# Kernel optimization log

Measured on AMD Instinct MI355X. Metric: run time of the kernel, lower is better.

The kernel has to match this reference:

```python
import jax, jax.numpy as jnp
import numpy as np

N_QUBITS = 8
N_LAYERS = 3
BN_EPS = 1e-5


def _apply_ry(state, theta, wire):
    # state: (B, 2, ..., 2) real statevector; theta: scalar or (B,)
    st = jnp.moveaxis(state, wire + 1, 1)
    t = jnp.asarray(theta, state.dtype)
    t = t.reshape(t.shape + (1,) * (state.ndim - 2))  # broadcast vs (B, 2^{n-1})
    c, s = jnp.cos(t / 2), jnp.sin(t / 2)
    s0, s1 = st[:, 0], st[:, 1]
    new = jnp.stack([c * s0 - s * s1, s * s0 + c * s1], axis=1)
    return jnp.moveaxis(new, 1, wire + 1)


def _apply_cnot(state, ctrl, tgt):
    # assumes ctrl < tgt (chain topology used by the circuit)
    st = jnp.moveaxis(state, ctrl + 1, 1)
    a0, a1 = st[:, 0], st[:, 1]
    a1 = jnp.flip(a1, axis=tgt)  # target axis is tgt after removing the ctrl axis
    new = jnp.stack([a0, a1], axis=1)
    return jnp.moveaxis(new, 1, ctrl + 1)


def _circuit(enc_angles, params):
    # Batched 8-qubit statevector simulation; RY/CNOT are real so the state is real.
    B = enc_angles.shape[0]
    state = jnp.zeros((B, 2 ** N_QUBITS), enc_angles.dtype).at[:, 0].set(1.0)
    state = state.reshape((B,) + (2,) * N_QUBITS)
    for i in range(4):  # feature-map encoder on first 4 wires
        state = _apply_ry(state, enc_angles[:, i], i)
    for layer in range(N_LAYERS):
        for q in range(N_QUBITS):
            state = _apply_ry(state, params[layer, q], q)
        for q in range(N_QUBITS - 1):
            state = _apply_cnot(state, q, q + 1)
    probs = state * state
    ez = []
    for w in range(N_QUBITS):
        axes = tuple(a for a in range(1, N_QUBITS + 1) if a != w + 1)
        p = probs.sum(axis=axes)  # (B, 2)
        ez.append(p[:, 0] - p[:, 1])  # <Z_w>
    return jnp.stack(ez, axis=-1)  # (B, N_QUBITS)


def setup_inputs() -> dict:
    key = jax.random.key(0)
    k1, k2, k3, k4 = jax.random.split(key, 4)
    B = 65536
    return {
        "x": jax.random.normal(k1, (B, 1, 12, 12), dtype=jnp.float32),
        "params": jax.random.normal(k2, (N_LAYERS, N_QUBITS), dtype=jnp.float32),
        "W": jax.random.normal(k3, (4, N_QUBITS), dtype=jnp.float32) * 0.3,
        "b": jax.random.normal(k4, (4,), dtype=jnp.float32) * 0.1,
        "gamma": jnp.ones((4,), dtype=jnp.float32),
        "beta": jnp.zeros((4,), dtype=jnp.float32),
    }


def reference(x, params, W, b, gamma, beta):
    B = x.shape[0]
    # avg_pool2d(kernel_size=6) on 12x12 -> 2x2, then flatten to 4 encoding angles
    pooled = x.reshape(B, 1, 2, 6, 2, 6).mean(axis=(3, 5)).reshape(B, 4)
    q_out = _circuit(pooled, params)          # (B, 8)
    out = q_out @ W.T + b                      # Linear(8 -> 4)
    mean = out.mean(axis=0)                    # BatchNorm1d training mode
    var = out.var(axis=0)                      # biased variance (torch BN)
    return gamma * (out - mean) / jnp.sqrt(var + BN_EPS) + beta
```

## Files before the change

### kernel.cpp

```cpp
#include <hip/hip_runtime.h>
#include <math.h>

#define NQ 8
#define NS 256
#define NK 16
#define NL 3
#define MTS 260

__global__ __launch_bounds__(256) void setup_kernel(
    const float* __restrict__ params,
    const float* __restrict__ W,
    float* __restrict__ R_ws,
    double* __restrict__ acc)
{
    __shared__ float M[NS * NK];
    __shared__ float MT[NK * MTS];
    __shared__ float PT[NK * MTS];
    const int t = threadIdx.x;
    const int j = blockIdx.x;

    if (j == 0) acc[t] = 0.0;

    #pragma unroll
    for (int k = 0; k < NK; ++k) M[t * NK + k] = 0.f;
    if ((t & 15) == 0) M[t * NK + (t >> 4)] = 1.f;

    const int pair = t & 127;
    const int kh   = t >> 7;

    for (int layer = 0; layer < NL; ++layer) {
        for (int q = 0; q < NQ; ++q) {
            __syncthreads();
            const float th = params[layer * 8 + q] * 0.5f;
            const float c  = __cosf(th);
            const float sn = __sinf(th);
            const int m   = 1 << (7 - q);
            const int low = pair & (m - 1);
            const int s0  = ((pair ^ low) << 1) | low;
            const int s1  = s0 | m;
            float v0[8], v1[8];
            #pragma unroll
            for (int k = 0; k < 8; ++k) {
                v0[k] = M[s0 * NK + kh * 8 + k];
                v1[k] = M[s1 * NK + kh * 8 + k];
            }
            #pragma unroll
            for (int k = 0; k < 8; ++k) {
                float n0 = c * v0[k] - sn * v1[k];
                float n1 = sn * v0[k] + c * v1[k];
                M[s0 * NK + kh * 8 + k] = n0;
                M[s1 * NK + kh * 8 + k] = n1;
            }
        }
        __syncthreads();
        int src = t;
        #pragma unroll
        for (int q = 6; q >= 0; --q) {
            int bit = (src >> (7 - q)) & 1;
            src ^= bit << (6 - q);
        }
        float r[NK];
        #pragma unroll
        for (int k = 0; k < NK; ++k) r[k] = M[src * NK + k];
        __syncthreads();
        #pragma unroll
        for (int k = 0; k < NK; ++k) M[t * NK + k] = r[k];
    }
    __syncthreads();

    {
        const int s = t;
        float ts = 0.f;
        #pragma unroll
        for (int w = 0; w < 8; ++w) {
            float sign = ((s >> (7 - w)) & 1) ? -1.f : 1.f;
            ts += W[j * 8 + w] * sign;
        }
        #pragma unroll
        for (int k = 0; k < NK; ++k) {
            float m = M[s * NK + k];
            MT[k * MTS + s] = m;
            PT[k * MTS + s] = ts * m;
        }
    }
    __syncthreads();

    const int k = t >> 4, l = t & 15;
    const float4* mk4 = (const float4*)&MT[k * MTS];
    const float4* pl4 = (const float4*)&PT[l * MTS];
    float r = 0.f;
    #pragma unroll 8
    for (int i = 0; i < NS / 4; ++i) {
        float4 a = mk4[i];
        float4 b = pl4[i];
        r += a.x * b.x + a.y * b.y + a.z * b.z + a.w * b.w;
    }
    R_ws[j * 256 + t] = r;
}

__global__ __launch_bounds__(256, 4) void main_kernel(
    const float* __restrict__ x,
    const float* __restrict__ bvec,
    const float* __restrict__ R_ws,
    float* __restrict__ out_col,
    double* __restrict__ acc,
    int B)
{
    __shared__ float4 tile[2304];
    __shared__ float  part[64 * 9];

    const int t   = threadIdx.x;
    const int blk = blockIdx.x;

    const float4* xg = (const float4*)x + (size_t)blk * 2304;
    #pragma unroll
    for (int i = 0; i < 9; ++i) tile[i * 256 + t] = xg[i * 256 + t];
    __syncthreads();

    {
        float sl = 0.f, sr = 0.f;
        #pragma unroll
        for (int i = 0; i < 9; ++i) {
            float4 v = tile[t * 9 + i];
            const int mod = i % 3;
            if (mod == 0)      { sl += v.x + v.y + v.z + v.w; }
            else if (mod == 1) { sl += v.x + v.y; sr += v.z + v.w; }
            else               { sr += v.x + v.y + v.z + v.w; }
        }
        part[(t >> 2) * 9 + (t & 3) * 2 + 0] = sl;
        part[(t >> 2) * 9 + (t & 3) * 2 + 1] = sr;
    }
    __syncthreads();

    const int e = t & 63;
    const int p = __builtin_amdgcn_readfirstlane(t >> 6);

    const float* pe = &part[e * 9];
    const float k36 = 0.5f / 36.f;
    float th0 = (pe[0] + pe[2]) * k36;
    float th1 = (pe[1] + pe[3]) * k36;
    float th2 = (pe[4] + pe[6]) * k36;
    float th3 = (pe[5] + pe[7]) * k36;

    float c0 = __cosf(th0), s0 = __sinf(th0);
    float c1 = __cosf(th1), s1 = __sinf(th1);
    float c2 = __cosf(th2), s2 = __sinf(th2);
    float c3 = __cosf(th3), s3 = __sinf(th3);

    float u[4] = { c0 * c1, c0 * s1, s0 * c1, s0 * s1 };
    float v[4] = { c2 * c3, c2 * s3, s2 * c3, s2 * s3 };
    float a[16];
    #pragma unroll
    for (int i = 0; i < 4; ++i)
        #pragma unroll
        for (int jj = 0; jj < 4; ++jj) a[i * 4 + jj] = u[i] * v[jj];

    const float* Rp = R_ws + p * 256;
    float o = bvec[p];
    #pragma unroll
    for (int kk = 0; kk < 16; ++kk) {
        float dot = 0.f;
        #pragma unroll
        for (int ll = 0; ll < 16; ++ll) dot = fmaf(Rp[kk * 16 + ll], a[ll], dot);
        o = fmaf(a[kk], dot, o);
    }

    out_col[(size_t)p * B + blk * 64 + e] = o;

    float s1v = o, s2v = o * o;
    #pragma unroll
    for (int off = 1; off < 64; off <<= 1) {
        s1v += __shfl_xor(s1v, off);
        s2v += __shfl_xor(s2v, off);
    }
    if (e == 0) {
        const int bin = blk & 31;
        atomicAdd(&acc[bin * 8 + p],     (double)s1v);
        atomicAdd(&acc[bin * 8 + 4 + p], (double)s2v);
    }
}

__global__ __launch_bounds__(256) void bn_kernel(
    const float* __restrict__ out_col,
    const double* __restrict__ acc,
    const float* __restrict__ gamma,
    const float* __restrict__ beta,
    float* __restrict__ outp,
    int B)
{
    __shared__ float sc[4], sh[4];
    const int t = threadIdx.x;
    if (t < 4) {
        double s = 0.0, s2 = 0.0;
        #pragma unroll
        for (int bin = 0; bin < 32; ++bin) {
            s  += acc[bin * 8 + t];
            s2 += acc[bin * 8 + 4 + t];
        }
        double invB = 1.0 / (double)B;
        double mean = s * invB;
        double var  = s2 * invB - mean * mean;
        float inv   = (float)(1.0 / sqrt(var + 1e-5));
        float g     = gamma[t] * inv;
        sc[t] = g;
        sh[t] = beta[t] - (float)mean * g;
    }
    __syncthreads();

    const int i = blockIdx.x * 256 + t;
    float o0 = out_col[(size_t)0 * B + i];
    float o1 = out_col[(size_t)1 * B + i];
    float o2 = out_col[(size_t)2 * B + i];
    float o3 = out_col[(size_t)3 * B + i];
    float4 r;
    r.x = fmaf(o0, sc[0], sh[0]);
    r.y = fmaf(o1, sc[1], sh[1]);
    r.z = fmaf(o2, sc[2], sh[2]);
    r.w = fmaf(o3, sc[3], sh[3]);
    ((float4*)outp)[i] = r;
}

extern "C" void kernel_launch(void* const* d_in, const int* in_sizes, int n_in,
                              void* d_out, int out_size, void* d_ws, size_t ws_size,
                              hipStream_t stream)
{
    const float* x      = (const float*)d_in[0];
    const float* params = (const float*)d_in[1];
    const float* W      = (const float*)d_in[2];
    const float* bvec   = (const float*)d_in[3];
    const float* gamma  = (const float*)d_in[4];
    const float* beta   = (const float*)d_in[5];

    const int B = in_sizes[0] / 144;

    float*  R_ws    = (float*)d_ws;
    double* acc     = (double*)((char*)d_ws + 4096);
    float*  out_col = (float*)((char*)d_ws + 8192);

    float* outp = (float*)d_out;

    setup_kernel<<<4, 256, 0, stream>>>(params, W, R_ws, acc);
    main_kernel<<<B / 64, 256, 0, stream>>>(x, bvec, R_ws, out_col, acc, B);
    bn_kernel<<<B / 256, 256, 0, stream>>>(out_col, acc, gamma, beta, outp, B);
}
```

Measured before the change: 110.0 us.

## Keep setup statevector rows in registers and apply RY gates via shuffles

The setup kernel now holds each basis state's 16-entry row in registers instead of shared memory. RY gates on low wires pair threads with cross-lane shuffles, and gates on the top two wires go through a padded shared buffer. This removes most shared-memory round trips and barriers in the gate loop. The final dot product is rewritten as explicit FMAs. The setup kernel is a tiny 4-block launch, so any effect on total time is likely small next to the main kernel.

New measurement: 103.9 us. 5.5% less time.

```diff
diff --git a/kernel.cpp b/kernel.cpp
--- a/kernel.cpp
+++ b/kernel.cpp
@@ -5,6 +5,7 @@
 #define NS 256
 #define NK 16
 #define NL 3
+#define XS 20
 #define MTS 260
 
 __global__ __launch_bounds__(256) void setup_kernel(
@@ -13,7 +14,7 @@
     float* __restrict__ R_ws,
     double* __restrict__ acc)
 {
-    __shared__ float M[NS * NK];
+    __shared__ float X[NS * XS];
     __shared__ float MT[NK * MTS];
     __shared__ float PT[NK * MTS];
     const int t = threadIdx.x;
@@ -21,67 +22,67 @@
 
     if (j == 0) acc[t] = 0.0;
 
-    #pragma unroll
-    for (int k = 0; k < NK; ++k) M[t * NK + k] = 0.f;
-    if ((t & 15) == 0) M[t * NK + (t >> 4)] = 1.f;
-
-    const int pair = t & 127;
-    const int kh   = t >> 7;
+    float m[NK];
+    #pragma unroll
+    for (int k = 0; k < NK; ++k) m[k] = 0.f;
+    if ((t & 15) == 0) m[t >> 4] = 1.f;
 
     for (int layer = 0; layer < NL; ++layer) {
         for (int q = 0; q < NQ; ++q) {
-            __syncthreads();
             const float th = params[layer * 8 + q] * 0.5f;
             const float c  = __cosf(th);
             const float sn = __sinf(th);
-            const int m   = 1 << (7 - q);
-            const int low = pair & (m - 1);
-            const int s0  = ((pair ^ low) << 1) | low;
-            const int s1  = s0 | m;
-            float v0[8], v1[8];
-            #pragma unroll
-            for (int k = 0; k < 8; ++k) {
-                v0[k] = M[s0 * NK + kh * 8 + k];
-                v1[k] = M[s1 * NK + kh * 8 + k];
+            const int mask = 1 << (7 - q);
+            const float ss = (t & mask) ? sn : -sn;
+            float p[NK];
+            if (mask >= 64) {
+                __syncthreads();
+                #pragma unroll
+                for (int k = 0; k < NK; k += 4)
+                    *(float4*)&X[t * XS + k] = make_float4(m[k], m[k+1], m[k+2], m[k+3]);
+                __syncthreads();
+                const int pt = t ^ mask;
+                #pragma unroll
+                for (int k = 0; k < NK; k += 4) {
+                    float4 v = *(const float4*)&X[pt * XS + k];
+                    p[k] = v.x; p[k+1] = v.y; p[k+2] = v.z; p[k+3] = v.w;
+                }
+            } else {
+                #pragma unroll
+                for (int k = 0; k < NK; ++k) p[k] = __shfl_xor(m[k], mask);
             }
             #pragma unroll
-            for (int k = 0; k < 8; ++k) {
-                float n0 = c * v0[k] - sn * v1[k];
-                float n1 = sn * v0[k] + c * v1[k];
-                M[s0 * NK + kh * 8 + k] = n0;
-                M[s1 * NK + kh * 8 + k] = n1;
-            }
-        }
-        __syncthreads();
+            for (int k = 0; k < NK; ++k) m[k] = fmaf(ss, p[k], c * m[k]);
+        }
         int src = t;
         #pragma unroll
         for (int q = 6; q >= 0; --q) {
             int bit = (src >> (7 - q)) & 1;
             src ^= bit << (6 - q);
         }
-        float r[NK];
-        #pragma unroll
-        for (int k = 0; k < NK; ++k) r[k] = M[src * NK + k];
         __syncthreads();
         #pragma unroll
-        for (int k = 0; k < NK; ++k) M[t * NK + k] = r[k];
-    }
-    __syncthreads();
-
-    {
-        const int s = t;
-        float ts = 0.f;
-        #pragma unroll
-        for (int w = 0; w < 8; ++w) {
-            float sign = ((s >> (7 - w)) & 1) ? -1.f : 1.f;
-            ts += W[j * 8 + w] * sign;
-        }
-        #pragma unroll
-        for (int k = 0; k < NK; ++k) {
-            float m = M[s * NK + k];
-            MT[k * MTS + s] = m;
-            PT[k * MTS + s] = ts * m;
-        }
+        for (int k = 0; k < NK; k += 4)
+            *(float4*)&X[t * XS + k] = make_float4(m[k], m[k+1], m[k+2], m[k+3]);
+        __syncthreads();
+        #pragma unroll
+        for (int k = 0; k < NK; k += 4) {
+            float4 v = *(const float4*)&X[src * XS + k];
+            m[k] = v.x; m[k+1] = v.y; m[k+2] = v.z; m[k+3] = v.w;
+        }
+    }
+
+    float ts = 0.f;
+    #pragma unroll
+    for (int w = 0; w < 8; ++w) {
+        float sign = ((t >> (7 - w)) & 1) ? -1.f : 1.f;
+        ts += W[j * 8 + w] * sign;
+    }
+
+    #pragma unroll
+    for (int k = 0; k < NK; ++k) {
+        MT[k * MTS + t] = m[k];
+        PT[k * MTS + t] = ts * m[k];
     }
     __syncthreads();
 
@@ -93,7 +94,10 @@
     for (int i = 0; i < NS / 4; ++i) {
         float4 a = mk4[i];
         float4 b = pl4[i];
-        r += a.x * b.x + a.y * b.y + a.z * b.z + a.w * b.w;
+        r = fmaf(a.x, b.x, r);
+        r = fmaf(a.y, b.y, r);
+        r = fmaf(a.z, b.z, r);
+        r = fmaf(a.w, b.w, r);
     }
     R_ws[j * 256 + t] = r;
 }
```
